# Optimization experiments

Hardware: AMD Instinct MI355X
Metric: run time of the kernel (lower is better)

The kernel has to match this reference:

```python
import jax, jax.numpy as jnp
import numpy as np

N_VERT = 1000          # num_of_vertices; x has 3*N_VERT rows
B = 32                 # batch
IN_DIM = 64
OUT_DIMS = [64, 64, 64]


def setup_inputs() -> dict:
    key = jax.random.key(0)
    ks = jax.random.split(key, 8)
    threeN = 3 * N_VERT
    x = jax.random.normal(ks[0], (threeN, B, IN_DIM), dtype=jnp.float32)
    # dense (normalized-ish) adjacency over the localized spatio-temporal graph
    adj = jax.random.uniform(ks[1], (threeN, threeN), dtype=jnp.float32) / threeN
    inp = {"x": x, "adj": adj}
    in_d = IN_DIM
    for i, out_d in enumerate(OUT_DIMS):
        # torch Linear(in_d, 2*out_d): store as [in_d, 2*out_d] for x @ W + b
        scale = 1.0 / np.sqrt(in_d)
        inp[f"W{i}"] = jax.random.uniform(ks[2 + 2 * i], (in_d, 2 * out_d),
                                          minval=-scale, maxval=scale, dtype=jnp.float32)
        inp[f"b{i}"] = jax.random.uniform(ks[3 + 2 * i], (2 * out_d,),
                                          minval=-scale, maxval=scale, dtype=jnp.float32)
        in_d = out_d
    return inp


def _gcn_glu(adj, x, W, b, out_dim):
    # aggregate: [3N,3N] x [3N,B,C] -> [3N,B,C]
    h = jnp.einsum('nm,mbc->nbc', adj, x)
    lr = h @ W + b                       # [3N,B,2*out]
    lhs, rhs = lr[..., :out_dim], lr[..., out_dim:]
    return lhs * jax.nn.sigmoid(rhs)     # GLU


def reference(x, adj, W0, b0, W1, b1, W2, b2):
    n = x.shape[0] // 3
    Ws = [(W0, b0), (W1, b1), (W2, b2)]
    mids = []
    h = x
    for (W, b), out_d in zip(Ws, OUT_DIMS):
        h = _gcn_glu(adj, h, W, b, out_d)
        mids.append(h[n:2 * n])          # middle time-step slice [N,B,out]
    return jnp.max(jnp.stack(mids, axis=0), axis=0)  # [N,B,out]
```

## Files before the change

### kernel.cpp

```cpp
#include <hip/hip_runtime.h>
#include <stdint.h>
#include <math.h>

#define NV   3000
#define MP   3072
#define NBC  2048
#define NMID 1000

typedef unsigned short u16;
typedef short  s8vec __attribute__((ext_vector_type(8)));
typedef float  f4vec __attribute__((ext_vector_type(4)));


__device__ __forceinline__ u16 f2b(float f) {
  union { float f; unsigned int u; } v; v.f = f;
  unsigned int r = v.u + 0x7FFFu + ((v.u >> 16) & 1u);
  return (u16)(r >> 16);
}
__device__ __forceinline__ float b2f(u16 u) {
  union { unsigned int u; float f; } v; v.u = ((unsigned int)u) << 16;
  return v.f;
}

__device__ __forceinline__ void gload16(const void* g, void* l) {
  __builtin_amdgcn_global_load_lds(
      (const __attribute__((address_space(1))) void*)g,
      (__attribute__((address_space(3))) void*)l, 16, 0, 0);
}

__global__ void k_conv(const float* __restrict__ adj,
                       const float* __restrict__ x,
                       const float* __restrict__ W0,
                       const float* __restrict__ W1,
                       const float* __restrict__ W2,
                       u16* __restrict__ adjt,
                       u16* __restrict__ xt,
                       u16* __restrict__ Wt) {
  __shared__ __align__(16) u16 tb[64][80];
  const int bid = blockIdx.x;
  const int t   = threadIdx.x;

  if (bid < 2304) {
    const int bx = bid % 48;
    const int by = bid / 48;
    {
      const int rl = t >> 2, quad = t & 3;
      const int r  = by * 64 + rl;
      const bool rok = (r < NV);
#pragma unroll
      for (int i = 0; i < 4; ++i) {
        int c = bx * 64 + quad * 16 + i * 4;
        float4 f = {0.f, 0.f, 0.f, 0.f};
        if (rok && c < NV) f = *(const float4*)(adj + (size_t)r * NV + c);
        ushort4 o;
        o.x = f2b(f.x); o.y = f2b(f.y); o.z = f2b(f.z); o.w = f2b(f.w);
        *(ushort4*)&tb[rl][quad * 16 + i * 4] = o;
      }
    }
    __syncthreads();
    {
#pragma unroll
      for (int h = 0; h < 2; ++h) {
        int chunk = t * 2 + h;
        int sel  = chunk >> 8;
        int g    = (chunk >> 6) & 3;
        int lane = chunk & 63;
        int row  = g * 16 + (lane & 15);
        int col  = sel * 32 + (lane >> 4) * 8;
        s8vec v = *(const s8vec*)&tb[row][col];
        size_t dst = ((size_t)(by * 96 + bx * 2 + sel) * 4 + g) * 512 + lane * 8;
        *(s8vec*)(adjt + dst) = v;
      }
    }
  } else if (bid < 3840) {
    const int r2 = bid - 2304;
    const int k0 = (r2 % 48) * 64;
    const int n0 = (r2 / 48) * 64;
    int kl = t >> 4, ch = t & 15;
#pragma unroll
    for (int r = 0; r < 4; ++r) {
      int k = k0 + kl + r * 16;
      float4 f = {0.f, 0.f, 0.f, 0.f};
      if (k < NV) f = *(const float4*)(x + (size_t)k * NBC + n0 + ch * 4);
      tb[ch * 4 + 0][kl + r * 16] = f2b(f.x);
      tb[ch * 4 + 1][kl + r * 16] = f2b(f.y);
      tb[ch * 4 + 2][kl + r * 16] = f2b(f.z);
      tb[ch * 4 + 3][kl + r * 16] = f2b(f.w);
    }
    __syncthreads();
    int nl = t >> 4, kc = t & 15;
#pragma unroll
    for (int r = 0; r < 4; ++r) {
      int n = n0 + nl + r * 16;
      int k = k0 + kc * 4;
      ushort4 o;
      o.x = tb[nl + r * 16][kc * 4 + 0];
      o.y = tb[nl + r * 16][kc * 4 + 1];
      o.z = tb[nl + r * 16][kc * 4 + 2];
      o.w = tb[nl + r * 16][kc * 4 + 3];
      int nt = n >> 7, g = (n >> 4) & 7, lr = n & 15;
      int kk = k >> 5, hi = (k >> 3) & 3, j = k & 7;
      size_t dst = ((size_t)(nt * 96 + kk) * 8 + g) * 512 +
                   (size_t)(hi * 16 + lr) * 8 + j;
      *(ushort4*)(xt + dst) = o;
    }
  } else {
    int e = (bid - 3840) * 256 + t;
    const float* W = (e < 8192) ? W0 : (e < 16384) ? W1 : W2;
    int r  = e & 8191;
    int kk = r >> 12, g = (r >> 9) & 7, ln = (r >> 3) & 63, jj = r & 7;
    int c = kk * 32 + (ln >> 4) * 8 + jj;
    int j = g * 16 + (ln & 15);
    Wt[e] = f2b(W[c * 128 + j]);
  }
}

template <int NKT>
__global__ __launch_bounds__(256, 3) void k_gemm(
    const u16* __restrict__ At,
    const u16* __restrict__ Xt,
    u16* __restrict__ Cbase,
    size_t cslot,
    int mtbase,
    int nmt,
    int crow0,
    int chunk) {
  __shared__ __align__(16) u16 S[3 * 8192];

  const int bid = blockIdx.x;
  const int swz = (bid & 7) * chunk + (bid >> 3);
  const int nt  = swz & 15;
  const int mk  = swz >> 4;
  const int ks  = mk / nmt;
  const int mt  = mk - ks * nmt;
  const int kt0 = ks * NKT;

  const int tid  = threadIdx.x;
  const int w    = tid >> 6;
  const int lane = tid & 63;
  const int wr   = w >> 1;
  const int wc   = w & 1;

  const int c0 = w * 4;
  const u16* src[4];
  int stp[4];
#pragma unroll
  for (int i = 0; i < 4; ++i) {
    int c = c0 + i;
    if (c < 8) {
      int m64 = (mtbase + mt) * 2 + (c >> 2);
      src[i] = At + ((size_t)(m64 * 96 + kt0) * 4 + (c & 3)) * 512 + lane * 8;
      stp[i] = 2048;
    } else {
      src[i] = Xt + ((size_t)(nt * 96 + kt0) * 8 + (c - 8)) * 512 + lane * 8;
      stp[i] = 4096;
    }
  }

  f4vec acc[4][4];
#pragma unroll
  for (int i = 0; i < 4; ++i)
#pragma unroll
    for (int j = 0; j < 4; ++j) acc[i][j] = (f4vec){0.f, 0.f, 0.f, 0.f};

  auto stage = [&](int buf, int s) {
    u16* d = S + buf * 8192 + c0 * 512;
#pragma unroll
    for (int i = 0; i < 4; ++i)
      gload16(src[i] + (size_t)s * stp[i], d + i * 512);
  };
  auto compute = [&](int buf) {
    const u16* Ab = S + buf * 8192 + (wr * 4) * 512 + lane * 8;
    const u16* Bb = S + buf * 8192 + 4096 + (wc * 4) * 512 + lane * 8;
    s8vec a[4], b[4];
#pragma unroll
    for (int mi = 0; mi < 4; ++mi)
      a[mi] = *(const s8vec*)(Ab + mi * 512);
#pragma unroll
    for (int ni = 0; ni < 4; ++ni)
      b[ni] = *(const s8vec*)(Bb + ni * 512);
    __builtin_amdgcn_s_setprio(1);
#pragma unroll
    for (int mi = 0; mi < 4; ++mi)
#pragma unroll
      for (int ni = 0; ni < 4; ++ni)
        acc[mi][ni] = __builtin_amdgcn_mfma_f32_16x16x32_bf16(
            a[mi], b[ni], acc[mi][ni], 0, 0, 0);
    __builtin_amdgcn_s_setprio(0);
  };

  stage(0, 0);
  stage(1, 1);

#pragma unroll 1
  for (int sb = 0; sb < NKT - 3; sb += 3) {
#pragma unroll
    for (int u = 0; u < 3; ++u) {
      const int s = sb + u;
      asm volatile("s_waitcnt vmcnt(4)" ::: "memory");
      asm volatile("s_barrier" ::: "memory");
      stage((u + 2) % 3, s + 2);
      compute(u);
    }
  }
  asm volatile("s_waitcnt vmcnt(4)" ::: "memory");
  asm volatile("s_barrier" ::: "memory");
  stage(2, NKT - 1);
  compute(0);
  asm volatile("s_waitcnt vmcnt(4)" ::: "memory");
  asm volatile("s_barrier" ::: "memory");
  compute(1);
  asm volatile("s_waitcnt vmcnt(0)" ::: "memory");
  asm volatile("s_barrier" ::: "memory");
  compute(2);

  u16* Cs = Cbase + (size_t)ks * cslot;
  const int rl = lane & 15;
  const int rh = lane >> 4;
  const int mrow0 = (mtbase + mt) * 128 + wr * 64 - crow0;
#pragma unroll
  for (int mi = 0; mi < 4; ++mi)
#pragma unroll
    for (int ni = 0; ni < 4; ++ni) {
      int grow = mrow0 + mi * 16 + rh * 4;
      int gcol = nt * 128 + wc * 64 + ni * 16 + rl;
      u16* cp = Cs + (size_t)grow * NBC + gcol;
      cp[0 * NBC] = f2b(acc[mi][ni][0]);
      cp[1 * NBC] = f2b(acc[mi][ni][1]);
      cp[2 * NBC] = f2b(acc[mi][ni][2]);
      cp[3 * NBC] = f2b(acc[mi][ni][3]);
    }
}

template <int LAYER0, int WRITEX>
__global__ __launch_bounds__(256) void k_layerB(
    const u16* __restrict__ H0,
    const u16* __restrict__ H1,
    const u16* __restrict__ Wt,
    const float* __restrict__ bias,
    u16* __restrict__ xt,
    float* __restrict__ out,
    int vt0) {
  __shared__ __align__(16) u16 Hs[2][2][8][64][8];

  const int vt = vt0 + blockIdx.x;
  const int b  = blockIdx.y;
  const int v0 = vt * 128;
  const int t  = threadIdx.x;

#pragma unroll
  for (int h = 0; h < 2; ++h) {
    const u16* H = h ? H1 : H0;
#pragma unroll
    for (int q = 0; q < 4; ++q) {
      int id = q * 256 + t;
      int v  = id >> 3;
      int cc = (id & 7) * 8;
      s8vec hh = *(const s8vec*)(H + (size_t)(v0 + v) * NBC + b * 64 + cc);
      int kk = cc >> 5, g = v >> 4, ln = ((cc >> 3) & 3) * 16 + (v & 15);
      *(s8vec*)&Hs[h][kk][g][ln][0] = hh;
    }
  }
  __syncthreads();

  const int w    = t >> 6;
  const int lane = t & 63;
  const int wvh  = w >> 1;
  const int wc   = w & 1;

  s8vec bf[4][2];
#pragma unroll
  for (int ni = 0; ni < 4; ++ni) {
    int g = (ni < 2) ? (wc * 2 + ni) : (4 + wc * 2 + (ni - 2));
#pragma unroll
    for (int kk = 0; kk < 2; ++kk)
      bf[ni][kk] = *(const s8vec*)(Wt + ((size_t)(kk * 8 + g) * 64 + lane) * 8);
  }

  f4vec acc[4][4];
#pragma unroll
  for (int i = 0; i < 4; ++i)
#pragma unroll
    for (int j = 0; j < 4; ++j) acc[i][j] = (f4vec){0.f, 0.f, 0.f, 0.f};

#pragma unroll
  for (int h = 0; h < 2; ++h)
#pragma unroll
    for (int kk = 0; kk < 2; ++kk) {
      s8vec a[4];
#pragma unroll
      for (int mi = 0; mi < 4; ++mi)
        a[mi] = *(const s8vec*)&Hs[h][kk][wvh * 4 + mi][lane][0];
#pragma unroll
      for (int mi = 0; mi < 4; ++mi)
#pragma unroll
        for (int ni = 0; ni < 4; ++ni)
          acc[mi][ni] = __builtin_amdgcn_mfma_f32_16x16x32_bf16(
              a[mi], bf[ni][kk], acc[mi][ni], 0, 0, 0);
    }

  const int lr = lane & 15;
  const int rh = lane >> 4;
#pragma unroll
  for (int mi = 0; mi < 4; ++mi) {
    const int vbase = v0 + wvh * 64 + mi * 16 + rh * 4;
#pragma unroll
    for (int np = 0; np < 2; ++np) {
      const int j  = wc * 32 + np * 16 + lr;
      const float bl = bias[j];
      const float bh = bias[j + 64];
      float vals[4];
#pragma unroll
      for (int r = 0; r < 4; ++r) {
        float lo = acc[mi][np][r] + bl;
        float hi = acc[mi][np + 2][r] + bh;
        float gv = lo / (1.0f + __expf(-hi));
        vals[r] = ((vbase + r) < NV) ? gv : 0.0f;
      }
#pragma unroll
      for (int r = 0; r < 4; ++r) {
        int vg = vbase + r;
        if (vg >= NMID && vg < 2 * NMID) {
          size_t oi = (size_t)(vg - NMID) * NBC + b * 64 + j;
          if (LAYER0) out[oi] = vals[r];
          else        out[oi] = fmaxf(out[oi], vals[r]);
        }
      }
      if (WRITEX) {
        int n   = b * 64 + j;
        int nt  = n >> 7, g2 = (n >> 4) & 7, ln2 = n & 15;
        int kk2 = vbase >> 5, hi2 = (vbase >> 3) & 3, jj0 = vbase & 7;
        ushort4 o;
        o.x = f2b(vals[0]); o.y = f2b(vals[1]);
        o.z = f2b(vals[2]); o.w = f2b(vals[3]);
        size_t dst = ((size_t)(nt * 96 + kk2) * 8 + g2) * 512 +
                     (size_t)(hi2 * 16 + ln2) * 8 + jj0;
        *(ushort4*)(xt + dst) = o;
      }
    }
  }
}

extern "C" void kernel_launch(void* const* d_in, const int* in_sizes, int n_in,
                              void* d_out, int out_size, void* d_ws, size_t ws_size,
                              hipStream_t stream) {
  const float* x   = (const float*)d_in[0];
  const float* adj = (const float*)d_in[1];
  const float* W0  = (const float*)d_in[2];
  const float* b0  = (const float*)d_in[3];
  const float* W1  = (const float*)d_in[4];
  const float* b1  = (const float*)d_in[5];
  const float* W2  = (const float*)d_in[6];
  const float* b2  = (const float*)d_in[7];
  float* out = (float*)d_out;

  char* ws = (char*)d_ws;
  u16* adjt = (u16*)ws;
  u16* xa   = (u16*)(ws + 18874368);
  u16* Hbuf = (u16*)(ws + 18874368 + 12582912);
  u16* Wt   = (u16*)(ws + 18874368 + 12582912 + 25165824);

  const size_t FS = (size_t)3072 * NBC;
  const size_t PS = (size_t)1152 * NBC;
  const size_t R0 = (size_t)896 * NBC;

  k_conv<<<3936, 256, 0, stream>>>(adj, x, W0, W1, W2, adjt, xa, Wt);

  k_gemm<48><<<768, 256, 0, stream>>>(adjt, xa, Hbuf, FS, 0, 24, 0, 96);
  k_layerB<1, 1><<<dim3(24, 32), 256, 0, stream>>>(
      Hbuf, Hbuf + FS, Wt, b0, xa, out, 0);
  k_gemm<48><<<768, 256, 0, stream>>>(adjt, xa, Hbuf, FS, 0, 24, 0, 96);
  k_layerB<0, 1><<<dim3(24, 32), 256, 0, stream>>>(
      Hbuf, Hbuf + FS, Wt + 8192, b1, xa, out, 0);
  k_gemm<48><<<288, 256, 0, stream>>>(adjt, xa, Hbuf, PS, 7, 9, 896, 36);
  k_layerB<0, 0><<<dim3(9, 32), 256, 0, stream>>>(
      Hbuf - R0, Hbuf + PS - R0, Wt + 16384, b2, xa, out, 7);
}
```

Measured before the change: 172.6 us.

## Use 192-row GEMM tiles with three-way split-K for full adjacency layers

```diff
diff --git a/kernel.cpp b/kernel.cpp
--- a/kernel.cpp
+++ b/kernel.cpp
@@ -115,6 +115,119 @@
   }
 }
 
+__global__ __launch_bounds__(256, 3) void k_gemm192(
+    const u16* __restrict__ At,
+    const u16* __restrict__ Xt,
+    u16* __restrict__ Cbase,
+    size_t cslot) {
+  __shared__ __align__(16) u16 S[3 * 6144 + 2 * 4096];
+
+  const int bid = blockIdx.x;
+  const int swz = (bid & 7) * 96 + (bid >> 3);
+  const int nt  = swz & 15;
+  const int mk  = swz >> 4;
+  const int ks  = mk >> 4;
+  const int mt  = mk & 15;
+  const int kt0 = ks * 32;
+
+  const int tid  = threadIdx.x;
+  const int w    = tid >> 6;
+  const int lane = tid & 63;
+  const int wr   = w >> 1;
+  const int wc   = w & 1;
+
+  const u16* asrc[3];
+#pragma unroll
+  for (int i = 0; i < 3; ++i) {
+    int c   = w * 3 + i;
+    int m64 = mt * 3 + (c >> 2);
+    asrc[i] = At + ((size_t)(m64 * 96 + kt0) * 4 + (c & 3)) * 512 + lane * 8;
+  }
+  const u16* bsrc[2];
+#pragma unroll
+  for (int i = 0; i < 2; ++i)
+    bsrc[i] = Xt + ((size_t)(nt * 96 + kt0) * 8 + (w * 2 + i)) * 512 + lane * 8;
+
+  f4vec acc[6][4];
+#pragma unroll
+  for (int i = 0; i < 6; ++i)
+#pragma unroll
+    for (int j = 0; j < 4; ++j) acc[i][j] = (f4vec){0.f, 0.f, 0.f, 0.f};
+
+  auto stageA = [&](int buf, int s) {
+    u16* d = S + buf * 6144 + (w * 3) * 512;
+#pragma unroll
+    for (int i = 0; i < 3; ++i)
+      gload16(asrc[i] + (size_t)s * 2048, d + i * 512);
+  };
+  auto stageB = [&](int buf, int s) {
+    u16* d = S + 18432 + buf * 4096 + (w * 2) * 512;
+#pragma unroll
+    for (int i = 0; i < 2; ++i)
+      gload16(bsrc[i] + (size_t)s * 4096, d + i * 512);
+  };
+  auto compute = [&](int ab, int bb) {
+    const u16* Ab = S + ab * 6144 + (wr * 6) * 512 + lane * 8;
+    const u16* Bb = S + 18432 + bb * 4096 + (wc * 4) * 512 + lane * 8;
+    s8vec a[6], b[4];
+#pragma unroll
+    for (int mi = 0; mi < 6; ++mi)
+      a[mi] = *(const s8vec*)(Ab + mi * 512);
+#pragma unroll
+    for (int ni = 0; ni < 4; ++ni)
+      b[ni] = *(const s8vec*)(Bb + ni * 512);
+    __builtin_amdgcn_s_setprio(1);
+#pragma unroll
+    for (int mi = 0; mi < 6; ++mi)
+#pragma unroll
+      for (int ni = 0; ni < 4; ++ni)
+        acc[mi][ni] = __builtin_amdgcn_mfma_f32_16x16x32_bf16(
+            a[mi], b[ni], acc[mi][ni], 0, 0, 0);
+    __builtin_amdgcn_s_setprio(0);
+  };
+
+  stageA(0, 0);
+  stageB(0, 0);
+  stageA(1, 1);
+
+#pragma unroll 1
+  for (int sb = 0; sb < 30; sb += 6) {
+#pragma unroll
+    for (int u = 0; u < 6; ++u) {
+      const int s = sb + u;
+      asm volatile("s_waitcnt vmcnt(3)" ::: "memory");
+      asm volatile("s_barrier" ::: "memory");
+      stageB((u + 1) & 1, s + 1);
+      stageA((u + 2) % 3, s + 2);
+      compute(u % 3, u & 1);
+    }
+  }
+  asm volatile("s_waitcnt vmcnt(3)" ::: "memory");
+  asm volatile("s_barrier" ::: "memory");
+  stageB(1, 31);
+  compute(0, 0);
+  asm volatile("s_waitcnt vmcnt(0)" ::: "memory");
+  asm volatile("s_barrier" ::: "memory");
+  compute(1, 1);
+
+  u16* Cs = Cbase + (size_t)ks * cslot;
+  const int rl = lane & 15;
+  const int rh = lane >> 4;
+  const int mrow0 = mt * 192 + wr * 96;
+#pragma unroll
+  for (int mi = 0; mi < 6; ++mi)
+#pragma unroll
+    for (int ni = 0; ni < 4; ++ni) {
+      int grow = mrow0 + mi * 16 + rh * 4;
+      int gcol = nt * 128 + wc * 64 + ni * 16 + rl;
+      u16* cp = Cs + (size_t)grow * NBC + gcol;
+      cp[0 * NBC] = f2b(acc[mi][ni][0]);
+      cp[1 * NBC] = f2b(acc[mi][ni][1]);
+      cp[2 * NBC] = f2b(acc[mi][ni][2]);
+      cp[3 * NBC] = f2b(acc[mi][ni][3]);
+    }
+}
+
 template <int NKT>
 __global__ __launch_bounds__(256, 3) void k_gemm(
     const u16* __restrict__ At,
@@ -232,25 +345,27 @@
     }
 }
 
-template <int LAYER0, int WRITEX>
+template <int LAYER0, int WRITEX, int NH>
 __global__ __launch_bounds__(256) void k_layerB(
     const u16* __restrict__ H0,
     const u16* __restrict__ H1,
+    const u16* __restrict__ H2,
     const u16* __restrict__ Wt,
     const float* __restrict__ bias,
     u16* __restrict__ xt,
     float* __restrict__ out,
     int vt0) {
-  __shared__ __align__(16) u16 Hs[2][2][8][64][8];
-
+  __shared__ __align__(16) u16 Hs[NH][2][8][64][8];
+
+  const u16* Hp[3] = {H0, H1, H2};
   const int vt = vt0 + blockIdx.x;
   const int b  = blockIdx.y;
   const int v0 = vt * 128;
   const int t  = threadIdx.x;
 
 #pragma unroll
-  for (int h = 0; h < 2; ++h) {
-    const u16* H = h ? H1 : H0;
+  for (int h = 0; h < NH; ++h) {
+    const u16* H = Hp[h];
 #pragma unroll
     for (int q = 0; q < 4; ++q) {
       int id = q * 256 + t;
@@ -284,7 +399,7 @@
     for (int j = 0; j < 4; ++j) acc[i][j] = (f4vec){0.f, 0.f, 0.f, 0.f};
 
 #pragma unroll
-  for (int h = 0; h < 2; ++h)
+  for (int h = 0; h < NH; ++h)
 #pragma unroll
     for (int kk = 0; kk < 2; ++kk) {
       s8vec a[4];
@@ -358,7 +473,7 @@
   u16* adjt = (u16*)ws;
   u16* xa   = (u16*)(ws + 18874368);
   u16* Hbuf = (u16*)(ws + 18874368 + 12582912);
-  u16* Wt   = (u16*)(ws + 18874368 + 12582912 + 25165824);
+  u16* Wt   = (u16*)(ws + 18874368 + 12582912 + 37748736);
 
   const size_t FS = (size_t)3072 * NBC;
   const size_t PS = (size_t)1152 * NBC;
@@ -366,13 +481,13 @@
 
   k_conv<<<3936, 256, 0, stream>>>(adj, x, W0, W1, W2, adjt, xa, Wt);
 
-  k_gemm<48><<<768, 256, 0, stream>>>(adjt, xa, Hbuf, FS, 0, 24, 0, 96);
-  k_layerB<1, 1><<<dim3(24, 32), 256, 0, stream>>>(
-      Hbuf, Hbuf + FS, Wt, b0, xa, out, 0);
-  k_gemm<48><<<768, 256, 0, stream>>>(adjt, xa, Hbuf, FS, 0, 24, 0, 96);
-  k_layerB<0, 1><<<dim3(24, 32), 256, 0, stream>>>(
-      Hbuf, Hbuf + FS, Wt + 8192, b1, xa, out, 0);
+  k_gemm192<<<768, 256, 0, stream>>>(adjt, xa, Hbuf, FS);
+  k_layerB<1, 1, 3><<<dim3(24, 32), 256, 0, stream>>>(
+      Hbuf, Hbuf + FS, Hbuf + 2 * FS, Wt, b0, xa, out, 0);
+  k_gemm192<<<768, 256, 0, stream>>>(adjt, xa, Hbuf, FS);
+  k_layerB<0, 1, 3><<<dim3(24, 32), 256, 0, stream>>>(
+      Hbuf, Hbuf + FS, Hbuf + 2 * FS, Wt + 8192, b1, xa, out, 0);
   k_gemm<48><<<288, 256, 0, stream>>>(adjt, xa, Hbuf, PS, 7, 9, 896, 36);
-  k_layerB<0, 0><<<dim3(9, 32), 256, 0, stream>>>(
-      Hbuf - R0, Hbuf + PS - R0, Wt + 16384, b2, xa, out, 7);
-}
+  k_layerB<0, 0, 2><<<dim3(9, 32), 256, 0, stream>>>(
+      Hbuf - R0, Hbuf + PS - R0, Hbuf, Wt + 16384, b2, xa, out, 7);
+}
```

New measurement: 177.3 us. 1.03x slower.

## Split final-layer K reduction four ways and sum partials in new epilogue kernel

Applied to the files above, without the earlier changes.

```diff
diff --git a/kernel.cpp b/kernel.cpp
--- a/kernel.cpp
+++ b/kernel.cpp
@@ -341,6 +341,84 @@
   }
 }
 
+__global__ __launch_bounds__(256) void k_layerB4(
+    const u16* __restrict__ H0, const u16* __restrict__ H1,
+    const u16* __restrict__ H2, const u16* __restrict__ H3,
+    const u16* __restrict__ Wt,
+    const float* __restrict__ bias,
+    float* __restrict__ out,
+    int vt0) {
+  const u16* Hp[4] = {H0, H1, H2, H3};
+  const int vt = vt0 + blockIdx.x;
+  const int b  = blockIdx.y;
+  const int v0 = vt * 128;
+  const int t  = threadIdx.x;
+
+  const int w    = t >> 6;
+  const int lane = t & 63;
+  const int wvh  = w >> 1;
+  const int wc   = w & 1;
+
+  s8vec bf[4][2];
+#pragma unroll
+  for (int ni = 0; ni < 4; ++ni) {
+    int g = (ni < 2) ? (wc * 2 + ni) : (4 + wc * 2 + (ni - 2));
+#pragma unroll
+    for (int kk = 0; kk < 2; ++kk)
+      bf[ni][kk] = *(const s8vec*)(Wt + ((size_t)(kk * 8 + g) * 64 + lane) * 8);
+  }
+
+  f4vec acc[4][4];
+#pragma unroll
+  for (int i = 0; i < 4; ++i)
+#pragma unroll
+    for (int j = 0; j < 4; ++j) acc[i][j] = (f4vec){0.f, 0.f, 0.f, 0.f};
+
+  const size_t fbase =
+      (size_t)(v0 + wvh * 64 + (lane & 15)) * NBC + b * 64 + (lane >> 4) * 8;
+#pragma unroll
+  for (int h = 0; h < 4; ++h) {
+    const u16* hp = Hp[h] + fbase;
+#pragma unroll
+    for (int kk = 0; kk < 2; ++kk) {
+      s8vec a[4];
+#pragma unroll
+      for (int mi = 0; mi < 4; ++mi)
+        a[mi] = *(const s8vec*)(hp + (size_t)(mi * 16) * NBC + kk * 32);
+#pragma unroll
+      for (int mi = 0; mi < 4; ++mi)
+#pragma unroll
+        for (int ni = 0; ni < 4; ++ni)
+          acc[mi][ni] = __builtin_amdgcn_mfma_f32_16x16x32_bf16(
+              a[mi], bf[ni][kk], acc[mi][ni], 0, 0, 0);
+    }
+  }
+
+  const int lr = lane & 15;
+  const int rh = lane >> 4;
+#pragma unroll
+  for (int mi = 0; mi < 4; ++mi) {
+    const int vbase = v0 + wvh * 64 + mi * 16 + rh * 4;
+#pragma unroll
+    for (int np = 0; np < 2; ++np) {
+      const int j  = wc * 32 + np * 16 + lr;
+      const float bl = bias[j];
+      const float bh = bias[j + 64];
+#pragma unroll
+      for (int r = 0; r < 4; ++r) {
+        float lo = acc[mi][np][r] + bl;
+        float hi = acc[mi][np + 2][r] + bh;
+        float gv = lo / (1.0f + __expf(-hi));
+        int vg = vbase + r;
+        if (vg >= NMID && vg < 2 * NMID) {
+          size_t oi = (size_t)(vg - NMID) * NBC + b * 64 + j;
+          out[oi] = fmaxf(out[oi], (vg < NV) ? gv : 0.0f);
+        }
+      }
+    }
+  }
+}
+
 extern "C" void kernel_launch(void* const* d_in, const int* in_sizes, int n_in,
                               void* d_out, int out_size, void* d_ws, size_t ws_size,
                               hipStream_t stream) {
@@ -372,7 +450,8 @@
   k_gemm<48><<<768, 256, 0, stream>>>(adjt, xa, Hbuf, FS, 0, 24, 0, 96);
   k_layerB<0, 1><<<dim3(24, 32), 256, 0, stream>>>(
       Hbuf, Hbuf + FS, Wt + 8192, b1, xa, out, 0);
-  k_gemm<48><<<288, 256, 0, stream>>>(adjt, xa, Hbuf, PS, 7, 9, 896, 36);
-  k_layerB<0, 0><<<dim3(9, 32), 256, 0, stream>>>(
-      Hbuf - R0, Hbuf + PS - R0, Wt + 16384, b2, xa, out, 7);
-}
+  k_gemm<24><<<576, 256, 0, stream>>>(adjt, xa, Hbuf, PS, 7, 9, 896, 72);
+  k_layerB4<<<dim3(9, 32), 256, 0, stream>>>(
+      Hbuf - R0, Hbuf + PS - R0, Hbuf + 2 * PS - R0, Hbuf + 3 * PS - R0,
+      Wt + 16384, b2, out, 7);
+}
```

New measurement: 178.0 us. +3.1%, slower.
